# Performance work log

Measured on AMD Instinct MI355X. Metric: run time of the kernel, lower is better.

## Reference

```python
import jax, jax.numpy as jnp
import numpy as np

B, L, D, R = 8, 2048, 512, 512  # batch, seq, feature, n_rules


def setup_inputs() -> dict:
    key = jax.random.key(0)
    ks = jax.random.split(key, 6)
    query = jax.random.normal(ks[0], (B, L, D), dtype=jnp.float32)
    # to_q: Linear(D, D)
    Wq = jax.random.normal(ks[1], (D, D), dtype=jnp.float32) / np.sqrt(D)
    bq = jnp.zeros((D,), dtype=jnp.float32)
    # to_c: Linear(L, R)
    Wc = jax.random.normal(ks[2], (R, L), dtype=jnp.float32) / np.sqrt(L)
    bc = jnp.zeros((R,), dtype=jnp.float32)
    # fuzzy rule params, torch.rand init (uniform [0,1)); widths kept away from 0
    centers = jax.random.uniform(ks[3], (R, D), dtype=jnp.float32)
    widths = jax.random.uniform(ks[4], (R, D), dtype=jnp.float32, minval=0.1, maxval=1.0)
    return {"query": query, "Wq": Wq, "bq": bq, "Wc": Wc, "bc": bc,
            "centers": centers, "widths": widths}


def reference(query, Wq, bq, Wc, bc, centers, widths):
    # q = to_q(query)  (projection=True)
    q = query @ Wq.T + bq  # (B, L, D)
    # z[b,l,r] = -0.5 * mean_d (|q - c| / w)^2 ; abs is a no-op under the square,
    # so expand (q - c)^2 / w^2 into three GEMM-friendly terms (exact same math).
    inv_w2 = 1.0 / (widths * widths)                      # (R, D)
    qq = (q * q) @ inv_w2.T                               # (B, L, R)
    qc = q @ (centers * inv_w2).T                         # (B, L, R)
    cc = jnp.sum(centers * centers * inv_w2, axis=-1)     # (R,)
    z = -(0.5 / D) * (qq - 2.0 * qc + cc)                 # (B, L, R)
    Fss = jax.nn.softmax(z, axis=-1)                      # (B, L, R); dropout p=0
    # conq = to_c applied along the L axis of query, yielding (B, R, D)
    conq = jnp.einsum('bld,rl->brd', query, Wc) + bc[None, :, None]
    return Fss @ conq                                     # (B, L, D)
```

## Files before the change

### kernel.cpp

```cpp
#include <hip/hip_runtime.h>
#include <hip/hip_bf16.h>

constexpr int Bb = 8, Ls = 2048, Dd = 512, Rr = 512;
constexpr int M1 = Bb * Ls;

typedef _Float16 h8v __attribute__((ext_vector_type(8)));
typedef _Float16 h4v __attribute__((ext_vector_type(4)));
typedef float f4v __attribute__((ext_vector_type(4)));

__device__ __forceinline__ void async_copy16(const void* g, void* l) {
  __builtin_amdgcn_global_load_lds((const __attribute__((address_space(1))) unsigned int*)g,
                                   (__attribute__((address_space(3))) unsigned int*)l, 16, 0, 0);
}

__global__ __launch_bounds__(256) void prep_all(
    const float* __restrict__ q, _Float16* __restrict__ qs, _Float16* __restrict__ qt,
    const float* __restrict__ Wq, _Float16* __restrict__ wq,
    const float* __restrict__ Wc, _Float16* __restrict__ wc,
    const float* __restrict__ centers, const float* __restrict__ widths,
    _Float16* __restrict__ iwh, _Float16* __restrict__ c2h, float* __restrict__ cc,
    float* __restrict__ rowsum) {
  const int bid = blockIdx.x, tid = threadIdx.x;
  if (bid < 2048) {
    __shared__ float t[64][65];
    const int b = bid >> 8;
    const int l0 = ((bid >> 3) & 31) * 64;
    const int d0 = (bid & 7) * 64;
    const int r = tid >> 4, c4 = (tid & 15) * 4;
#pragma unroll
    for (int i = 0; i < 4; ++i) {
      const int l = r + i * 16;
      const float4 v = *(const float4*)&q[((long)b * Ls + l0 + l) * Dd + d0 + c4];
      t[l][c4] = v.x; t[l][c4 + 1] = v.y; t[l][c4 + 2] = v.z; t[l][c4 + 3] = v.w;
      h4v h = {(_Float16)v.x, (_Float16)v.y, (_Float16)v.z, (_Float16)v.w};
      *(h4v*)&qs[((long)b * Ls + l0 + l) * Dd + d0 + c4] = h;
    }
    __syncthreads();
#pragma unroll
    for (int i = 0; i < 4; ++i) {
      const int d = r + i * 16;
      h4v h = {(_Float16)t[c4][d], (_Float16)t[c4 + 1][d],
               (_Float16)t[c4 + 2][d], (_Float16)t[c4 + 3][d]};
      *(h4v*)&qt[((long)b * Dd + d0 + d) * Ls + l0 + c4] = h;
    }
  } else if (bid < 2304) {
    const int i = (bid - 2048) * 256 + tid;
    float4 v = *(const float4*)&Wq[(long)i * 4];
    h4v o = {(_Float16)v.x, (_Float16)v.y, (_Float16)v.z, (_Float16)v.w};
    *(h4v*)&wq[(long)i * 4] = o;
  } else if (bid < 3328) {
    const int i = (bid - 2304) * 256 + tid;
    float4 v = *(const float4*)&Wc[(long)i * 4];
    h4v o = {(_Float16)v.x, (_Float16)v.y, (_Float16)v.z, (_Float16)v.w};
    *(h4v*)&wc[(long)i * 4] = o;
  } else if (bid < 3456) {
    const int wave = tid >> 6, lane = tid & 63;
    const int r = (bid - 3328) * 4 + wave;
    float s = 0.f;
#pragma unroll
    for (int j = 0; j < 8; ++j) {
      const int d = j * 64 + lane;
      const float c = centers[(long)r * Dd + d];
      const float w = widths[(long)r * Dd + d];
      const float iw = 1.0f / (w * w);
      iwh[(long)r * Dd + d] = (_Float16)iw;
      c2h[(long)r * Dd + d] = (_Float16)(-2.0f * c * iw);
      s += c * c * iw;
    }
#pragma unroll
    for (int o = 32; o > 0; o >>= 1) s += __shfl_xor(s, o, 64);
    if (lane == 0) cc[r] = s;
  } else {
    const int i = (bid - 3456) * 256 + tid;
    ((float4*)rowsum)[i] = (float4){0.f, 0.f, 0.f, 0.f};
  }
}

template <int WM, int EPI>
__device__ __forceinline__ void gemm_body(
    const int lin, const int NX, const int NY, _Float16* __restrict__ smem,
    const _Float16* __restrict__ A, const _Float16* __restrict__ Bm,
    const float* __restrict__ bias, float* __restrict__ Cf, _Float16* __restrict__ Ch,
    const int Kext, const int ldA, const int ldB, const int ldC, const int kstep,
    const long sA, const long sB, const long sC) {
  constexpr int TM = WM * 32;
  _Float16* As = smem;
  _Float16* Bs = smem + TM * 64;

  const int xcd = lin & 7;
  const int wi = lin >> 3;
  const int x = wi % NX;
  const int yy = (wi / NX) * 8 + xcd;
  const int y = yy % NY;
  const int zz = yy / NY;
  const int n0 = x * 128;
  const int m0 = y * TM;
  const int kb = zz * kstep;
  const _Float16* Ab = A + (long)zz * sA;
  const _Float16* Bbp = Bm + (long)zz * sB;

  const int tid = threadIdx.x;
  const int wave = tid >> 6, lane = tid & 63;
  const int wm = wave >> 2, wn = wave & 3;
  const int quad = lane >> 4, tr = lane & 15;
  const int lrow = lane >> 2;
  const int lcol = (lane & 3) * 8;

  f4v acc[WM][2];
#pragma unroll
  for (int i = 0; i < WM; ++i)
#pragma unroll
    for (int j = 0; j < 2; ++j) acc[i][j] = (f4v){0.f, 0.f, 0.f, 0.f};

  for (int k0 = 0; k0 < Kext; k0 += 64) {
    __syncthreads();
#pragma unroll
    for (int c = wave; c < TM / 16; c += 8) {
      const long g = (long)(m0 + c * 16 + lrow) * ldA + kb + k0 + lcol;
      async_copy16(Ab + g, &As[c * 512]);
      async_copy16(Ab + g + 32, &As[TM * 32 + c * 512]);
    }
#pragma unroll
    for (int c = wave; c < 8; c += 8) {
      const long g = (long)(n0 + c * 16 + lrow) * ldB + kb + k0 + lcol;
      async_copy16(Bbp + g, &Bs[c * 512]);
      async_copy16(Bbp + g + 32, &Bs[4096 + c * 512]);
    }
    __syncthreads();

#pragma unroll
    for (int h = 0; h < 2; ++h) {
      h8v af[WM], bf[2];
#pragma unroll
      for (int i = 0; i < WM; ++i)
        af[i] = *(const h8v*)&As[h * (TM * 32) + (wm * (WM * 16) + i * 16 + tr) * 32 + quad * 8];
#pragma unroll
      for (int j = 0; j < 2; ++j)
        bf[j] = *(const h8v*)&Bs[h * 4096 + (wn * 32 + j * 16 + tr) * 32 + quad * 8];
#pragma unroll
      for (int i = 0; i < WM; ++i)
#pragma unroll
        for (int j = 0; j < 2; ++j)
          acc[i][j] = __builtin_amdgcn_mfma_f32_16x16x32_f16(af[i], bf[j], acc[i][j], 0, 0, 0);
    }
  }

  float* Cfb = Cf ? Cf + (long)zz * sC : nullptr;
  _Float16* Chb = Ch ? Ch + (long)zz * sC : nullptr;
#pragma unroll
  for (int i = 0; i < WM; ++i) {
    const int rbase = m0 + wm * (WM * 16) + i * 16 + quad * 4;
    float inv[4];
    if (EPI == 4) {
#pragma unroll
      for (int r = 0; r < 4; ++r) inv[r] = 1.0f / bias[(long)zz * Ls + rbase + r];
    }
#pragma unroll
    for (int j = 0; j < 2; ++j) {
      const int cg = n0 + wn * 32 + j * 16 + tr;
#pragma unroll
      for (int r = 0; r < 4; ++r) {
        const float v = acc[i][j][r];
        const long row = rbase + r;
        if (EPI == 2) {
          Chb[row * (long)ldC + cg] = (_Float16)(v + bias[cg]);
        } else if (EPI == 3) {
          Cfb[row * (long)ldC + cg] = v;
        } else if (EPI == 4) {
          Cfb[row * (long)ldC + cg] = v * inv[r];
        }
      }
    }
  }
}

template <int WM, int EPI>
__global__ __launch_bounds__(512, 4) void gemm_h(
    const _Float16* __restrict__ A, const _Float16* __restrict__ Bm,
    const float* __restrict__ bias, float* __restrict__ Cf,
    _Float16* __restrict__ Ch, int Kext, int ldA, int ldB, int ldC, int kstep,
    long sA, long sB, long sC) {
  extern __shared__ _Float16 smem[];
  const int lin = ((int)blockIdx.z * (int)gridDim.y + (int)blockIdx.y) * (int)gridDim.x +
                  (int)blockIdx.x;
  gemm_body<WM, EPI>(lin, (int)gridDim.x, (int)gridDim.y, smem, A, Bm, bias, Cf, Ch,
                     Kext, ldA, ldB, ldC, kstep, sA, sB, sC);
}

__global__ __launch_bounds__(512, 4) void qgemm_conq(
    const _Float16* __restrict__ qs, const _Float16* __restrict__ wq,
    const float* __restrict__ bq, _Float16* __restrict__ q16,
    const _Float16* __restrict__ qt, const _Float16* __restrict__ wc,
    const float* __restrict__ bc, _Float16* __restrict__ cq) {
  extern __shared__ _Float16 smem[];
  const int bid = (int)blockIdx.x;
  if (bid < 256) {
    gemm_body<2, 2>(bid, 4, 64, smem, qt, wc, bc, nullptr, cq,
                    Ls, Ls, Ls, Rr, 0, 0, 0, 0);
  } else {
    gemm_body<4, 2>(bid - 256, 4, 128, smem, qs, wq, bq, nullptr, q16,
                    Dd, Dd, Dd, Dd, 0, 0, 0, 0);
  }
}

__global__ __launch_bounds__(512, 4) void zq_gemm(
    const _Float16* __restrict__ Q, const _Float16* __restrict__ Iw,
    const _Float16* __restrict__ C2, const float* __restrict__ cc,
    _Float16* __restrict__ Fh, float* __restrict__ rowsum) {
  __shared__ _Float16 As[2][128 * 32];
  __shared__ _Float16 B1[2][128 * 32];
  __shared__ _Float16 B2[2][128 * 32];
  __shared__ float rowpart[128][4];
  const int lin = (int)blockIdx.y * 4 + (int)blockIdx.x;
  const int xcd = lin & 7;
  const int wi = lin >> 3;
  const int x = wi % 4;
  const int yy = (wi / 4) * 8 + xcd;
  const int n0 = x * 128;
  const int m0 = yy * 128;

  const int tid = threadIdx.x;
  const int wave = tid >> 6, lane = tid & 63;
  const int wm = wave >> 2, wn = wave & 3;
  const int quad = lane >> 4, tr = lane & 15;
  const int lrow = lane >> 2;
  const int lcol = (lane & 3) * 8;

  f4v acc[4][2];
#pragma unroll
  for (int i = 0; i < 4; ++i)
#pragma unroll
    for (int j = 0; j < 2; ++j) acc[i][j] = (f4v){0.f, 0.f, 0.f, 0.f};

  for (int k0 = 0; k0 < 512; k0 += 64) {
    __syncthreads();
    {
      const long ga = (long)(m0 + wave * 16 + lrow) * 512 + k0 + lcol;
      async_copy16(Q + ga, &As[0][wave * 512]);
      async_copy16(Q + ga + 32, &As[1][wave * 512]);
      const long gb = (long)(n0 + wave * 16 + lrow) * 512 + k0 + lcol;
      async_copy16(Iw + gb, &B1[0][wave * 512]);
      async_copy16(Iw + gb + 32, &B1[1][wave * 512]);
      async_copy16(C2 + gb, &B2[0][wave * 512]);
      async_copy16(C2 + gb + 32, &B2[1][wave * 512]);
    }
    __syncthreads();

#pragma unroll
    for (int h = 0; h < 2; ++h) {
      h8v af[4], af2[4], b1[2], b2[2];
#pragma unroll
      for (int i = 0; i < 4; ++i) {
        af[i] = *(const h8v*)&As[h][(wm * 64 + i * 16 + tr) * 32 + quad * 8];
        af2[i] = af[i] * af[i];
      }
#pragma unroll
      for (int j = 0; j < 2; ++j) {
        b1[j] = *(const h8v*)&B1[h][(wn * 32 + j * 16 + tr) * 32 + quad * 8];
        b2[j] = *(const h8v*)&B2[h][(wn * 32 + j * 16 + tr) * 32 + quad * 8];
      }
#pragma unroll
      for (int i = 0; i < 4; ++i)
#pragma unroll
        for (int j = 0; j < 2; ++j) {
          acc[i][j] = __builtin_amdgcn_mfma_f32_16x16x32_f16(af2[i], b1[j], acc[i][j], 0, 0, 0);
          acc[i][j] = __builtin_amdgcn_mfma_f32_16x16x32_f16(af[i], b2[j], acc[i][j], 0, 0, 0);
        }
    }
  }

  constexpr float zs = -0.0009765625f;
#pragma unroll
  for (int i = 0; i < 4; ++i) {
    float ps[2][4];
#pragma unroll
    for (int j = 0; j < 2; ++j) {
      const int cg = n0 + wn * 32 + j * 16 + tr;
      const float ccv = cc[cg];
#pragma unroll
      for (int r = 0; r < 4; ++r) ps[j][r] = __expf((acc[i][j][r] + ccv) * zs);
    }
    const int rbase = m0 + wm * 64 + i * 16 + quad * 4;
#pragma unroll
    for (int j = 0; j < 2; ++j) {
      const int cg = n0 + wn * 32 + j * 16 + tr;
#pragma unroll
      for (int r = 0; r < 4; ++r)
        Fh[(long)(rbase + r) * 512 + cg] = (_Float16)ps[j][r];
    }
#pragma unroll
    for (int r = 0; r < 4; ++r) {
      float s = ps[0][r] + ps[1][r];
#pragma unroll
      for (int o = 8; o > 0; o >>= 1) s += __shfl_xor(s, o, 64);
      if (tr == 0) rowpart[wm * 64 + i * 16 + quad * 4 + r][wn] = s;
    }
  }
  __syncthreads();
  if (tid < 128) {
    const float s = rowpart[tid][0] + rowpart[tid][1] + rowpart[tid][2] + rowpart[tid][3];
    atomicAdd(&rowsum[m0 + tid], s);
  }
}

extern "C" void kernel_launch(void* const* d_in, const int* in_sizes, int n_in,
                              void* d_out, int out_size, void* d_ws, size_t ws_size,
                              hipStream_t stream) {
  const float* query   = (const float*)d_in[0];
  const float* Wq      = (const float*)d_in[1];
  const float* bq      = (const float*)d_in[2];
  const float* Wc      = (const float*)d_in[3];
  const float* bc      = (const float*)d_in[4];
  const float* centers = (const float*)d_in[5];
  const float* widths  = (const float*)d_in[6];
  float* out = (float*)d_out;

  char* base = (char*)d_ws;
  auto alloc = [&](size_t bytes) {
    char* p = base;
    base += (bytes + 255) & ~(size_t)255;
    return p;
  };
  _Float16* qs  = (_Float16*)alloc((size_t)M1 * Dd * 2);
  _Float16* qt  = (_Float16*)alloc((size_t)M1 * Dd * 2);
  _Float16* q16 = (_Float16*)alloc((size_t)M1 * Dd * 2);
  _Float16* fs  = (_Float16*)alloc((size_t)M1 * Rr * 2);
  _Float16* wq  = (_Float16*)alloc((size_t)Dd * Dd * 2);
  _Float16* wc  = (_Float16*)alloc((size_t)Rr * Ls * 2);
  _Float16* iwh = (_Float16*)alloc((size_t)Rr * Dd * 2);
  _Float16* c2h = (_Float16*)alloc((size_t)Rr * Dd * 2);
  float*    cc  = (float*)alloc((size_t)Rr * 4);
  float*    rowsum = (float*)alloc((size_t)M1 * 4);
  _Float16* cq  = (_Float16*)alloc((size_t)Bb * Dd * Rr * 2);

  prep_all<<<3472, 256, 0, stream>>>(query, qs, qt, Wq, wq, Wc, wc,
                                     centers, widths, iwh, c2h, cc, rowsum);

  qgemm_conq<<<768, 512, 32768, stream>>>(qs, wq, bq, q16, qt, wc, bc, cq);

  zq_gemm<<<dim3(Rr / 128, M1 / 128, 1), 512, 0, stream>>>(q16, iwh, c2h, cc, fs, rowsum);

  gemm_h<4, 4><<<dim3(Dd / 128, Ls / 128, Bb), 512, 32768, stream>>>(
      fs, cq, rowsum, out, nullptr, Rr, Rr, Rr, Dd, 0,
      (long)Ls * Rr, (long)Dd * Rr, (long)Ls * Dd);
}
```

Baseline: 163.8 us.

## Double-buffer LDS k-halves so async loads overlap MFMA compute in GEMM kernels

Both GEMM main loops now split each 64-wide k-step into two 32-wide halves held in separate LDS stages. The load of the next half is issued before computing on the current one, so global-to-LDS async copies overlap the MFMA work instead of running in strict load, sync, compute phases. This hides memory latency at the cost of finer-grained synchronisation, with a barrier per 32-k step. The global_load_lds copies must complete before the barrier for correctness.

```diff
diff --git a/kernel.cpp b/kernel.cpp
--- a/kernel.cpp
+++ b/kernel.cpp
@@ -112,37 +112,41 @@
 #pragma unroll
     for (int j = 0; j < 2; ++j) acc[i][j] = (f4v){0.f, 0.f, 0.f, 0.f};
 
-  for (int k0 = 0; k0 < Kext; k0 += 64) {
-    __syncthreads();
+  auto stage = [&](const int s, const int kk) {
 #pragma unroll
     for (int c = wave; c < TM / 16; c += 8) {
-      const long g = (long)(m0 + c * 16 + lrow) * ldA + kb + k0 + lcol;
-      async_copy16(Ab + g, &As[c * 512]);
-      async_copy16(Ab + g + 32, &As[TM * 32 + c * 512]);
-    }
-#pragma unroll
-    for (int c = wave; c < 8; c += 8) {
-      const long g = (long)(n0 + c * 16 + lrow) * ldB + kb + k0 + lcol;
-      async_copy16(Bbp + g, &Bs[c * 512]);
-      async_copy16(Bbp + g + 32, &Bs[4096 + c * 512]);
-    }
-    __syncthreads();
-
-#pragma unroll
-    for (int h = 0; h < 2; ++h) {
-      h8v af[WM], bf[2];
-#pragma unroll
-      for (int i = 0; i < WM; ++i)
-        af[i] = *(const h8v*)&As[h * (TM * 32) + (wm * (WM * 16) + i * 16 + tr) * 32 + quad * 8];
+      const long g = (long)(m0 + c * 16 + lrow) * ldA + kb + kk + lcol;
+      async_copy16(Ab + g, &As[s * (TM * 32) + c * 512]);
+    }
+    {
+      const long g = (long)(n0 + wave * 16 + lrow) * ldB + kb + kk + lcol;
+      async_copy16(Bbp + g, &Bs[s * 4096 + wave * 512]);
+    }
+  };
+  auto compute = [&](const int s) {
+    h8v af[WM], bf[2];
+#pragma unroll
+    for (int i = 0; i < WM; ++i)
+      af[i] = *(const h8v*)&As[s * (TM * 32) + (wm * (WM * 16) + i * 16 + tr) * 32 + quad * 8];
+#pragma unroll
+    for (int j = 0; j < 2; ++j)
+      bf[j] = *(const h8v*)&Bs[s * 4096 + (wn * 32 + j * 16 + tr) * 32 + quad * 8];
+#pragma unroll
+    for (int i = 0; i < WM; ++i)
 #pragma unroll
       for (int j = 0; j < 2; ++j)
-        bf[j] = *(const h8v*)&Bs[h * 4096 + (wn * 32 + j * 16 + tr) * 32 + quad * 8];
-#pragma unroll
-      for (int i = 0; i < WM; ++i)
-#pragma unroll
-        for (int j = 0; j < 2; ++j)
-          acc[i][j] = __builtin_amdgcn_mfma_f32_16x16x32_f16(af[i], bf[j], acc[i][j], 0, 0, 0);
-    }
+        acc[i][j] = __builtin_amdgcn_mfma_f32_16x16x32_f16(af[i], bf[j], acc[i][j], 0, 0, 0);
+  };
+
+  stage(0, 0);
+  __syncthreads();
+  for (int kk = 0; kk < Kext; kk += 64) {
+    if (kk + 32 < Kext) stage(1, kk + 32);
+    compute(0);
+    __syncthreads();
+    if (kk + 64 < Kext) stage(0, kk + 64);
+    compute(1);
+    __syncthreads();
   }
 
   float* Cfb = Cf ? Cf + (long)zz * sC : nullptr;
@@ -232,41 +236,43 @@
 #pragma unroll
     for (int j = 0; j < 2; ++j) acc[i][j] = (f4v){0.f, 0.f, 0.f, 0.f};
 
-  for (int k0 = 0; k0 < 512; k0 += 64) {
-    __syncthreads();
-    {
-      const long ga = (long)(m0 + wave * 16 + lrow) * 512 + k0 + lcol;
-      async_copy16(Q + ga, &As[0][wave * 512]);
-      async_copy16(Q + ga + 32, &As[1][wave * 512]);
-      const long gb = (long)(n0 + wave * 16 + lrow) * 512 + k0 + lcol;
-      async_copy16(Iw + gb, &B1[0][wave * 512]);
-      async_copy16(Iw + gb + 32, &B1[1][wave * 512]);
-      async_copy16(C2 + gb, &B2[0][wave * 512]);
-      async_copy16(C2 + gb + 32, &B2[1][wave * 512]);
-    }
-    __syncthreads();
-
-#pragma unroll
-    for (int h = 0; h < 2; ++h) {
-      h8v af[4], af2[4], b1[2], b2[2];
-#pragma unroll
-      for (int i = 0; i < 4; ++i) {
-        af[i] = *(const h8v*)&As[h][(wm * 64 + i * 16 + tr) * 32 + quad * 8];
-        af2[i] = af[i] * af[i];
+  auto stage = [&](const int s, const int kk) {
+    const long ga = (long)(m0 + wave * 16 + lrow) * 512 + kk + lcol;
+    async_copy16(Q + ga, &As[s][wave * 512]);
+    const long gb = (long)(n0 + wave * 16 + lrow) * 512 + kk + lcol;
+    async_copy16(Iw + gb, &B1[s][wave * 512]);
+    async_copy16(C2 + gb, &B2[s][wave * 512]);
+  };
+  auto compute = [&](const int s) {
+    h8v af[4], af2[4], b1[2], b2[2];
+#pragma unroll
+    for (int i = 0; i < 4; ++i) {
+      af[i] = *(const h8v*)&As[s][(wm * 64 + i * 16 + tr) * 32 + quad * 8];
+      af2[i] = af[i] * af[i];
+    }
+#pragma unroll
+    for (int j = 0; j < 2; ++j) {
+      b1[j] = *(const h8v*)&B1[s][(wn * 32 + j * 16 + tr) * 32 + quad * 8];
+      b2[j] = *(const h8v*)&B2[s][(wn * 32 + j * 16 + tr) * 32 + quad * 8];
+    }
+#pragma unroll
+    for (int i = 0; i < 4; ++i)
+#pragma unroll
+      for (int j = 0; j < 2; ++j) {
+        acc[i][j] = __builtin_amdgcn_mfma_f32_16x16x32_f16(af2[i], b1[j], acc[i][j], 0, 0, 0);
+        acc[i][j] = __builtin_amdgcn_mfma_f32_16x16x32_f16(af[i], b2[j], acc[i][j], 0, 0, 0);
       }
-#pragma unroll
-      for (int j = 0; j < 2; ++j) {
-        b1[j] = *(const h8v*)&B1[h][(wn * 32 + j * 16 + tr) * 32 + quad * 8];
-        b2[j] = *(const h8v*)&B2[h][(wn * 32 + j * 16 + tr) * 32 + quad * 8];
-      }
-#pragma unroll
-      for (int i = 0; i < 4; ++i)
-#pragma unroll
-        for (int j = 0; j < 2; ++j) {
-          acc[i][j] = __builtin_amdgcn_mfma_f32_16x16x32_f16(af2[i], b1[j], acc[i][j], 0, 0, 0);
-          acc[i][j] = __builtin_amdgcn_mfma_f32_16x16x32_f16(af[i], b2[j], acc[i][j], 0, 0, 0);
-        }
-    }
+  };
+
+  stage(0, 0);
+  __syncthreads();
+  for (int kk = 0; kk < 512; kk += 64) {
+    if (kk + 32 < 512) stage(1, kk + 32);
+    compute(0);
+    __syncthreads();
+    if (kk + 64 < 512) stage(0, kk + 64);
+    compute(1);
+    __syncthreads();
   }
 
   constexpr float zs = -0.0009765625f;
```

New measurement: 175.2 us. +6.9%, slower.

## Switch generic GEMMs to 4-wave 128x128 tiles with 64x64 per-wave subtiles

Applied to the files above, without the earlier changes.

Restructures the shared GEMM body from 8 waves (512 threads) with 32-column per-wave tiles to 4 waves (256 threads), each computing a 64x64 subtile with 4x4 MFMA accumulators. The conq GEMM grows its tile from 64 to 128 rows, halving its block count, and the unused kstep/split-K parameter is removed. The aim is more MFMA work per LDS fragment load and fewer blocks to schedule. In exchange it uses more accumulator registers per thread, lowers occupancy (launch bounds 256,3), and reduces parallelism for the conq GEMM.

```diff
diff --git a/kernel.cpp b/kernel.cpp
--- a/kernel.cpp
+++ b/kernel.cpp
@@ -76,16 +76,15 @@
   }
 }
 
-template <int WM, int EPI>
+template <int EPI>
 __device__ __forceinline__ void gemm_body(
     const int lin, const int NX, const int NY, _Float16* __restrict__ smem,
     const _Float16* __restrict__ A, const _Float16* __restrict__ Bm,
     const float* __restrict__ bias, float* __restrict__ Cf, _Float16* __restrict__ Ch,
-    const int Kext, const int ldA, const int ldB, const int ldC, const int kstep,
+    const int Kext, const int ldA, const int ldB, const int ldC,
     const long sA, const long sB, const long sC) {
-  constexpr int TM = WM * 32;
   _Float16* As = smem;
-  _Float16* Bs = smem + TM * 64;
+  _Float16* Bs = smem + 8192;
 
   const int xcd = lin & 7;
   const int wi = lin >> 3;
@@ -94,53 +93,49 @@
   const int y = yy % NY;
   const int zz = yy / NY;
   const int n0 = x * 128;
-  const int m0 = y * TM;
-  const int kb = zz * kstep;
+  const int m0 = y * 128;
   const _Float16* Ab = A + (long)zz * sA;
   const _Float16* Bbp = Bm + (long)zz * sB;
 
   const int tid = threadIdx.x;
   const int wave = tid >> 6, lane = tid & 63;
-  const int wm = wave >> 2, wn = wave & 3;
+  const int wm = wave >> 1, wn = wave & 1;
   const int quad = lane >> 4, tr = lane & 15;
   const int lrow = lane >> 2;
   const int lcol = (lane & 3) * 8;
 
-  f4v acc[WM][2];
-#pragma unroll
-  for (int i = 0; i < WM; ++i)
-#pragma unroll
-    for (int j = 0; j < 2; ++j) acc[i][j] = (f4v){0.f, 0.f, 0.f, 0.f};
+  f4v acc[4][4];
+#pragma unroll
+  for (int i = 0; i < 4; ++i)
+#pragma unroll
+    for (int j = 0; j < 4; ++j) acc[i][j] = (f4v){0.f, 0.f, 0.f, 0.f};
 
   for (int k0 = 0; k0 < Kext; k0 += 64) {
     __syncthreads();
 #pragma unroll
-    for (int c = wave; c < TM / 16; c += 8) {
-      const long g = (long)(m0 + c * 16 + lrow) * ldA + kb + k0 + lcol;
-      async_copy16(Ab + g, &As[c * 512]);
-      async_copy16(Ab + g + 32, &As[TM * 32 + c * 512]);
-    }
-#pragma unroll
-    for (int c = wave; c < 8; c += 8) {
-      const long g = (long)(n0 + c * 16 + lrow) * ldB + kb + k0 + lcol;
-      async_copy16(Bbp + g, &Bs[c * 512]);
-      async_copy16(Bbp + g + 32, &Bs[4096 + c * 512]);
+    for (int c = wave; c < 8; c += 4) {
+      const long ga = (long)(m0 + c * 16 + lrow) * ldA + k0 + lcol;
+      async_copy16(Ab + ga, &As[c * 512]);
+      async_copy16(Ab + ga + 32, &As[4096 + c * 512]);
+      const long gb = (long)(n0 + c * 16 + lrow) * ldB + k0 + lcol;
+      async_copy16(Bbp + gb, &Bs[c * 512]);
+      async_copy16(Bbp + gb + 32, &Bs[4096 + c * 512]);
     }
     __syncthreads();
 
 #pragma unroll
     for (int h = 0; h < 2; ++h) {
-      h8v af[WM], bf[2];
-#pragma unroll
-      for (int i = 0; i < WM; ++i)
-        af[i] = *(const h8v*)&As[h * (TM * 32) + (wm * (WM * 16) + i * 16 + tr) * 32 + quad * 8];
-#pragma unroll
-      for (int j = 0; j < 2; ++j)
-        bf[j] = *(const h8v*)&Bs[h * 4096 + (wn * 32 + j * 16 + tr) * 32 + quad * 8];
-#pragma unroll
-      for (int i = 0; i < WM; ++i)
-#pragma unroll
-        for (int j = 0; j < 2; ++j)
+      h8v af[4], bf[4];
+#pragma unroll
+      for (int i = 0; i < 4; ++i)
+        af[i] = *(const h8v*)&As[h * 4096 + (wm * 64 + i * 16 + tr) * 32 + quad * 8];
+#pragma unroll
+      for (int j = 0; j < 4; ++j)
+        bf[j] = *(const h8v*)&Bs[h * 4096 + (wn * 64 + j * 16 + tr) * 32 + quad * 8];
+#pragma unroll
+      for (int i = 0; i < 4; ++i)
+#pragma unroll
+        for (int j = 0; j < 4; ++j)
           acc[i][j] = __builtin_amdgcn_mfma_f32_16x16x32_f16(af[i], bf[j], acc[i][j], 0, 0, 0);
     }
   }
@@ -148,16 +143,16 @@
   float* Cfb = Cf ? Cf + (long)zz * sC : nullptr;
   _Float16* Chb = Ch ? Ch + (long)zz * sC : nullptr;
 #pragma unroll
-  for (int i = 0; i < WM; ++i) {
-    const int rbase = m0 + wm * (WM * 16) + i * 16 + quad * 4;
+  for (int i = 0; i < 4; ++i) {
+    const int rbase = m0 + wm * 64 + i * 16 + quad * 4;
     float inv[4];
     if (EPI == 4) {
 #pragma unroll
       for (int r = 0; r < 4; ++r) inv[r] = 1.0f / bias[(long)zz * Ls + rbase + r];
     }
 #pragma unroll
-    for (int j = 0; j < 2; ++j) {
-      const int cg = n0 + wn * 32 + j * 16 + tr;
+    for (int j = 0; j < 4; ++j) {
+      const int cg = n0 + wn * 64 + j * 16 + tr;
 #pragma unroll
       for (int r = 0; r < 4; ++r) {
         const float v = acc[i][j][r];
@@ -174,32 +169,32 @@
   }
 }
 
-template <int WM, int EPI>
-__global__ __launch_bounds__(512, 4) void gemm_h(
+template <int EPI>
+__global__ __launch_bounds__(256, 3) void gemm_h(
     const _Float16* __restrict__ A, const _Float16* __restrict__ Bm,
     const float* __restrict__ bias, float* __restrict__ Cf,
-    _Float16* __restrict__ Ch, int Kext, int ldA, int ldB, int ldC, int kstep,
+    _Float16* __restrict__ Ch, int Kext, int ldA, int ldB, int ldC,
     long sA, long sB, long sC) {
   extern __shared__ _Float16 smem[];
   const int lin = ((int)blockIdx.z * (int)gridDim.y + (int)blockIdx.y) * (int)gridDim.x +
                   (int)blockIdx.x;
-  gemm_body<WM, EPI>(lin, (int)gridDim.x, (int)gridDim.y, smem, A, Bm, bias, Cf, Ch,
-                     Kext, ldA, ldB, ldC, kstep, sA, sB, sC);
-}
-
-__global__ __launch_bounds__(512, 4) void qgemm_conq(
+  gemm_body<EPI>(lin, (int)gridDim.x, (int)gridDim.y, smem, A, Bm, bias, Cf, Ch,
+                 Kext, ldA, ldB, ldC, sA, sB, sC);
+}
+
+__global__ __launch_bounds__(256, 3) void qgemm_conq(
     const _Float16* __restrict__ qs, const _Float16* __restrict__ wq,
     const float* __restrict__ bq, _Float16* __restrict__ q16,
     const _Float16* __restrict__ qt, const _Float16* __restrict__ wc,
     const float* __restrict__ bc, _Float16* __restrict__ cq) {
   extern __shared__ _Float16 smem[];
   const int bid = (int)blockIdx.x;
-  if (bid < 256) {
-    gemm_body<2, 2>(bid, 4, 64, smem, qt, wc, bc, nullptr, cq,
-                    Ls, Ls, Ls, Rr, 0, 0, 0, 0);
+  if (bid < 128) {
+    gemm_body<2>(bid, 4, 32, smem, qt, wc, bc, nullptr, cq,
+                 Ls, Ls, Ls, Rr, 0, 0, 0);
   } else {
-    gemm_body<4, 2>(bid - 256, 4, 128, smem, qs, wq, bq, nullptr, q16,
-                    Dd, Dd, Dd, Dd, 0, 0, 0, 0);
+    gemm_body<2>(bid - 128, 4, 128, smem, qs, wq, bq, nullptr, q16,
+                 Dd, Dd, Dd, Dd, 0, 0, 0);
   }
 }
 
@@ -336,11 +331,11 @@
   prep_all<<<3472, 256, 0, stream>>>(query, qs, qt, Wq, wq, Wc, wc,
                                      centers, widths, iwh, c2h, cc, rowsum);
 
-  qgemm_conq<<<768, 512, 32768, stream>>>(qs, wq, bq, q16, qt, wc, bc, cq);
+  qgemm_conq<<<640, 256, 32768, stream>>>(qs, wq, bq, q16, qt, wc, bc, cq);
 
   zq_gemm<<<dim3(Rr / 128, M1 / 128, 1), 512, 0, stream>>>(q16, iwh, c2h, cc, fs, rowsum);
 
-  gemm_h<4, 4><<<dim3(Dd / 128, Ls / 128, Bb), 512, 32768, stream>>>(
-      fs, cq, rowsum, out, nullptr, Rr, Rr, Rr, Dd, 0,
+  gemm_h<4><<<dim3(Dd / 128, Ls / 128, Bb), 256, 32768, stream>>>(
+      fs, cq, rowsum, out, nullptr, Rr, Rr, Rr, Dd,
       (long)Ls * Rr, (long)Dd * Rr, (long)Ls * Dd);
 }
```

Measured after the change: 174.1 us. +6.3%, slower.
